# Kernel tuning notes

Measured on AMD Instinct MI355X. Metric: run time of the kernel, lower is better.

The kernel has to match this reference:

```python
import jax, jax.numpy as jnp
import numpy as np

DIM, SEQ, HEADS, HDIM, BATCH, VOCAB, NVOCAB = 512, 1024, 8, 64, 8, 1024, 3
EPS = 1e-5


def layer_norm(x, g, b):
    mu = x.mean(-1, keepdims=True)
    var = x.var(-1, keepdims=True)
    return (x - mu) * jax.lax.rsqrt(var + EPS) * g + b


def multiscale_retention(x, Wq, Wk, Wv, Wg, Wo):
    B, S, D = x.shape
    def split(h):  # [B,S,D] -> [B,H,S,hd]
        return h.reshape(B, S, HEADS, HDIM).transpose(0, 2, 1, 3)
    q, k, v = split(x @ Wq), split(x @ Wk), split(x @ Wv)
    # RetNet per-head decays and causal decay matrix D[h,n,m] = gamma_h^(n-m), n>=m
    gammas = 1.0 - 2.0 ** (-5.0 - jnp.arange(HEADS, dtype=jnp.float32))
    n = jnp.arange(S)
    diff = n[:, None] - n[None, :]
    decay = jnp.where(diff >= 0, gammas[:, None, None] ** jnp.maximum(diff, 0).astype(jnp.float32), 0.0)
    scores = jnp.einsum('bhsd,bhtd->bhst', q, k) * (1.0 / np.sqrt(HDIM))
    y = jnp.einsum('bhst,bhtd->bhsd', scores * decay, v)
    # group norm per head (no affine)
    mu = y.mean(-1, keepdims=True)
    var = y.var(-1, keepdims=True)
    y = (y - mu) * jax.lax.rsqrt(var + EPS)
    y = y.transpose(0, 2, 1, 3).reshape(B, S, D)
    gate = jax.nn.swish(x @ Wg)
    return (gate * y) @ Wo


def feed_forward(x, W1, b1, W2, b2):
    return jax.nn.relu(x @ W1 + b1) @ W2 + b2


def setup_inputs() -> dict:
    key = jax.random.key(0)
    ks = jax.random.split(key, 12)
    s = 0.02
    return {
        'ids': jax.random.randint(ks[0], (NVOCAB, BATCH, SEQ), 0, VOCAB),
        'emb_tables': jax.random.normal(ks[1], (NVOCAB, VOCAB, DIM), jnp.float32) * s,
        'pos_emb': jax.random.normal(ks[2], (NVOCAB, SEQ, DIM), jnp.float32) * s,
        'ln_gamma': jnp.ones((DIM,), jnp.float32),
        'ln_beta': jnp.zeros((DIM,), jnp.float32),
        'Wq': jax.random.normal(ks[3], (DIM, DIM), jnp.float32) * s,
        'Wk': jax.random.normal(ks[4], (DIM, DIM), jnp.float32) * s,
        'Wv': jax.random.normal(ks[5], (DIM, DIM), jnp.float32) * s,
        'Wg': jax.random.normal(ks[6], (DIM, DIM), jnp.float32) * s,
        'Wo': jax.random.normal(ks[7], (DIM, DIM), jnp.float32) * s,
        'W1': jax.random.normal(ks[8], (DIM, DIM), jnp.float32) * s,
        'b1': jnp.zeros((DIM,), jnp.float32),
        'W2': jax.random.normal(ks[9], (DIM, DIM), jnp.float32) * s,
        'b2': jnp.zeros((DIM,), jnp.float32),
        'fc_W': jax.random.normal(ks[10], (SEQ * DIM, 1), jnp.float32) * s,
        'fc_b': jnp.zeros((1,), jnp.float32),
    }


def reference(ids, emb_tables, pos_emb, ln_gamma, ln_beta, Wq, Wk, Wv, Wg, Wo,
              W1, b1, W2, b2, fc_W, fc_b):
    x = None
    for i in range(NVOCAB):  # loop over vocab embeddings, x overwritten each pass (as in source)
        emb = emb_tables[i][ids[i]] + pos_emb[i][None, :, :]  # [B,S,D]
        x = layer_norm(emb, ln_gamma, ln_beta)
        x = multiscale_retention(x, Wq, Wk, Wv, Wg, Wo) + x
        x = feed_forward(layer_norm(x, ln_gamma, ln_beta), W1, b1, W2, b2) + x
        x = layer_norm(x, ln_gamma, ln_beta)
    flat = x.reshape(x.shape[0], -1)  # Flatten
    return jax.nn.sigmoid(flat @ fc_W + fc_b)  # dropout inactive at inference
```

## Files before the change

### kernel.cpp

```cpp
#include <hip/hip_runtime.h>
#include <math.h>

typedef unsigned short u16;
typedef __attribute__((ext_vector_type(8))) _Float16 half8;
typedef __attribute__((ext_vector_type(4))) float f32x4;
typedef __attribute__((ext_vector_type(4))) unsigned short us4;


static __device__ __forceinline__ u16 f2h(float f) {
    _Float16 h = (_Float16)f;
    return __builtin_bit_cast(u16, h);
}
static __device__ __forceinline__ float h2f(u16 u) {
    return (float)__builtin_bit_cast(_Float16, u);
}
static __device__ __forceinline__ void gl_lds16(const void* g, void* l) {
    __builtin_amdgcn_global_load_lds(
        (const __attribute__((address_space(1))) void*)g,
        (__attribute__((address_space(3))) void*)l, 16, 0, 0);
}

__global__ __launch_bounds__(256) void prep_kernel(
    const float* __restrict__ Wq, const float* __restrict__ Wk, const float* __restrict__ Wv,
    const float* __restrict__ Wg, const float* __restrict__ Wo, const float* __restrict__ W1,
    const float* __restrict__ W2, u16* __restrict__ WT,
    const int* __restrict__ ids, const float* __restrict__ emb, const float* __restrict__ pos,
    const float* __restrict__ gam, const float* __restrict__ bet, u16* __restrict__ x0h)
{
    __shared__ float tile[64][65];
    int bx = blockIdx.x, t = threadIdx.x;
    if (bx < 448) {
        const float* Ws[7] = {Wq, Wk, Wv, Wg, Wo, W1, W2};
        int w = bx >> 6, rem = bx & 63;
        int k0 = (rem >> 3) * 64, n0 = (rem & 7) * 64;
        const float* W = Ws[w];
        for (int c = t; c < 4096; c += 256) {
            int row = c >> 6, col = c & 63;
            tile[row][col] = W[(size_t)(k0 + row) * 512 + n0 + col];
        }
        __syncthreads();
        for (int c = t; c < 4096; c += 256) {
            int row = c >> 6, col = c & 63;
            WT[(size_t)w * 262144 + (size_t)(n0 + row) * 512 + k0 + col] = f2h(tile[col][row]);
        }
    } else {
        int wid = t >> 6, lane = t & 63;
        int row = (bx - 448) * 4 + wid;
        int col = lane * 8;
        int id = ids[2 * 8192 + row];
        const float* e = emb + (size_t)(2 * 1024 + id) * 512 + col;
        const float* p = pos + (size_t)(2 * 1024 + (row & 1023)) * 512 + col;
        float4 e0 = *(const float4*)e, e1 = *(const float4*)(e + 4);
        float4 p0 = *(const float4*)p, p1 = *(const float4*)(p + 4);
        float v[8] = {e0.x + p0.x, e0.y + p0.y, e0.z + p0.z, e0.w + p0.w,
                      e1.x + p1.x, e1.y + p1.y, e1.z + p1.z, e1.w + p1.w};
        float s1 = 0.f, s2 = 0.f;
#pragma unroll
        for (int j = 0; j < 8; ++j) { s1 += v[j]; s2 += v[j] * v[j]; }
#pragma unroll
        for (int o = 32; o >= 1; o >>= 1) {
            s1 += __shfl_xor(s1, o, 64);
            s2 += __shfl_xor(s2, o, 64);
        }
        float mu = s1 * (1.f / 512.f);
        float var = fmaxf(s2 * (1.f / 512.f) - mu * mu, 0.f);
        float rs = 1.f / sqrtf(var + 1e-5f);
        float4 g0 = *(const float4*)&gam[col], g1 = *(const float4*)&gam[col + 4];
        float4 b0 = *(const float4*)&bet[col], b1 = *(const float4*)&bet[col + 4];
        float gv[8] = {g0.x, g0.y, g0.z, g0.w, g1.x, g1.y, g1.z, g1.w};
        float bv[8] = {b0.x, b0.y, b0.z, b0.w, b1.x, b1.y, b1.z, b1.w};
        half8 hv;
#pragma unroll
        for (int j = 0; j < 8; ++j) hv[j] = (_Float16)((v[j] - mu) * rs * gv[j] + bv[j]);
        *(half8*)&x0h[(size_t)row * 512 + col] = hv;
    }
}

__global__ __launch_bounds__(256) void ln_kernel(
    const u16* __restrict__ xin,
    const float* __restrict__ gam, const float* __restrict__ bet,
    u16* __restrict__ outh,
    const float* __restrict__ fcW, float* __restrict__ fcpart)
{
    int wid = threadIdx.x >> 6, lane = threadIdx.x & 63;
    int row = blockIdx.x * 4 + wid;
    int col = lane * 8;
    float v[8];
    half8 x = *(const half8*)&xin[(size_t)row * 512 + col];
#pragma unroll
    for (int j = 0; j < 8; ++j) v[j] = (float)x[j];
    float s1 = 0.f, s2 = 0.f;
#pragma unroll
    for (int j = 0; j < 8; ++j) { s1 += v[j]; s2 += v[j] * v[j]; }
#pragma unroll
    for (int o = 32; o >= 1; o >>= 1) {
        s1 += __shfl_xor(s1, o, 64);
        s2 += __shfl_xor(s2, o, 64);
    }
    float mu = s1 * (1.f / 512.f);
    float var = fmaxf(s2 * (1.f / 512.f) - mu * mu, 0.f);
    float rs = 1.f / sqrtf(var + 1e-5f);
    float4 g0 = *(const float4*)&gam[col], g1 = *(const float4*)&gam[col + 4];
    float4 b0 = *(const float4*)&bet[col], b1 = *(const float4*)&bet[col + 4];
    float gv[8] = {g0.x, g0.y, g0.z, g0.w, g1.x, g1.y, g1.z, g1.w};
    float bv[8] = {b0.x, b0.y, b0.z, b0.w, b1.x, b1.y, b1.z, b1.w};
    float y[8];
#pragma unroll
    for (int j = 0; j < 8; ++j) y[j] = (v[j] - mu) * rs * gv[j] + bv[j];
    if (outh) {
        half8 hv;
#pragma unroll
        for (int j = 0; j < 8; ++j) hv[j] = (_Float16)y[j];
        *(half8*)&outh[(size_t)row * 512 + col] = hv;
    }
    if (fcW) {
        int srow = row & 1023;
        const float* wp = &fcW[(size_t)srow * 512 + col];
        float4 w0 = *(const float4*)wp, w1 = *(const float4*)(wp + 4);
        float d = y[0] * w0.x + y[1] * w0.y + y[2] * w0.z + y[3] * w0.w +
                  y[4] * w1.x + y[5] * w1.y + y[6] * w1.z + y[7] * w1.w;
#pragma unroll
        for (int o = 32; o >= 1; o >>= 1) d += __shfl_xor(d, o, 64);
        if (lane == 0) fcpart[row] = d;
    }
}

static __device__ __forceinline__ void stage_tile(
    const u16* pa0, const u16* pa1, const u16* pb0, const u16* pb1,
    u16* ldsw, int slot, int kt)
{
    int off = kt * 32;
    u16* d = ldsw + slot * 16384;
    gl_lds16(pa0 + off, d);
    gl_lds16(pa1 + off, d + 4096);
    gl_lds16(pb0 + off, d + 8192);
    gl_lds16(pb1 + off, d + 12288);
}

static __device__ __forceinline__ void compute_tile(
    const u16* lds, int slot, int wm, int wn, int quad, int l15, f32x4 (&acc)[8][4])
{
    const u16* A = lds + slot * 16384;
    const u16* B = A + 8192;
    __builtin_amdgcn_s_setprio(1);
#pragma unroll
    for (int mq = 0; mq < 2; ++mq)
#pragma unroll
        for (int nq = 0; nq < 2; ++nq) {
            half8 a[4], b[2];
#pragma unroll
            for (int i = 0; i < 4; ++i)
                a[i] = *(const half8*)&A[(wm * 128 + mq * 64 + i * 16 + l15) * 32 + quad * 8];
#pragma unroll
            for (int j = 0; j < 2; ++j)
                b[j] = *(const half8*)&B[(wn * 64 + nq * 32 + j * 16 + l15) * 32 + quad * 8];
#pragma unroll
            for (int i = 0; i < 4; ++i)
#pragma unroll
                for (int j = 0; j < 2; ++j)
                    acc[mq * 4 + i][nq * 2 + j] = __builtin_amdgcn_mfma_f32_16x16x32_f16(
                        a[i], b[j], acc[mq * 4 + i][nq * 2 + j], 0, 0, 0);
        }
    __builtin_amdgcn_s_setprio(0);
}

#define QITER(KT, VM)                                                              \
    do {                                                                           \
        if ((KT) + 3 < 16) stage_tile(pa0, pa1, pb0, pb1, ldsw, ((KT) + 3) & 3, (KT) + 3); \
        asm volatile("s_waitcnt vmcnt(" #VM ")" ::: "memory");                     \
        __builtin_amdgcn_s_barrier();                                              \
        asm volatile("" ::: "memory");                                             \
        compute_tile(lds, (KT) & 3, wm, wn, quad, l15, acc);                       \
        asm volatile("" ::: "memory");                                             \
        __builtin_amdgcn_s_barrier();                                              \
    } while (0)

__global__ __launch_bounds__(512, 2) void gemm_f16(
    const u16* __restrict__ A2, const u16* __restrict__ Bg,
    u16* __restrict__ outh, int ostride)
{
    __shared__ u16 lds[65536];
    int t = threadIdx.x;
    int wid = t >> 6, lane = t & 63, quad = lane >> 4, l15 = lane & 15;
    int wm = wid >> 2, wn = wid & 3;
    int orig = blockIdx.x;
    int wgid = (orig & 7) * 32 + (orig >> 3);
    int m0 = (wgid >> 3) * 256, n0 = (wgid & 7) * 256;

    int srow = t >> 2, sc = (t & 3) * 8;
    const u16* pa0 = A2 + (size_t)(m0 + srow) * 512 + sc;
    const u16* pa1 = pa0 + (size_t)128 * 512;
    const u16* pb0 = Bg + (size_t)(n0 + srow) * 512 + sc;
    const u16* pb1 = pb0 + (size_t)128 * 512;
    u16* ldsw = lds + wid * 512;

    f32x4 acc[8][4];
#pragma unroll
    for (int i = 0; i < 8; ++i)
#pragma unroll
        for (int j = 0; j < 4; ++j) acc[i][j] = (f32x4){0.f, 0.f, 0.f, 0.f};

    stage_tile(pa0, pa1, pb0, pb1, ldsw, 0, 0);
    stage_tile(pa0, pa1, pb0, pb1, ldsw, 1, 1);
    stage_tile(pa0, pa1, pb0, pb1, ldsw, 2, 2);

    QITER(0, 12);  QITER(1, 12);  QITER(2, 12);  QITER(3, 12);
    QITER(4, 12);  QITER(5, 12);  QITER(6, 12);  QITER(7, 12);
    QITER(8, 12);  QITER(9, 12);  QITER(10, 12); QITER(11, 12);
    QITER(12, 12);
    QITER(13, 8);  QITER(14, 4);  QITER(15, 0);

    u16* C = lds;
#pragma unroll
    for (int i = 0; i < 8; ++i)
#pragma unroll
        for (int j = 0; j < 4; ++j)
#pragma unroll
            for (int r = 0; r < 4; ++r)
                C[(wm * 128 + i * 16 + quad * 4 + r) * 256 + wn * 64 + j * 16 + l15] =
                    f2h(acc[i][j][r]);
    __builtin_amdgcn_s_barrier();
    asm volatile("" ::: "memory");
#pragma unroll
    for (int it = 0; it < 16; ++it) {
        int idx = it * 512 + t;
        int row = idx >> 5, ch = idx & 31;
        *(half8*)&outh[(size_t)(m0 + row) * ostride + n0 + ch * 8] =
            *(const half8*)&C[row * 256 + ch * 8];
    }
}

static __device__ __forceinline__ void stage_n64(
    const u16* pa, const u16* pb, u16* ldsw, int slot, int kt)
{
    int off = kt * 32;
    u16* d = ldsw + slot * 8192;
    gl_lds16(pa + off, d);
    gl_lds16(pb + off, d + 4096);
}

static __device__ __forceinline__ void compute_n64(
    const u16* lds, int slot, int wm, int wn, int quad, int l15, f32x4 (&acc)[4][2])
{
    const u16* A = lds + slot * 8192;
    const u16* B = A + 4096;
    __builtin_amdgcn_s_setprio(1);
    half8 a[4], b[2];
#pragma unroll
    for (int i = 0; i < 4; ++i)
        a[i] = *(const half8*)&A[(wm * 64 + i * 16 + l15) * 32 + quad * 8];
#pragma unroll
    for (int j = 0; j < 2; ++j)
        b[j] = *(const half8*)&B[(wn * 32 + j * 16 + l15) * 32 + quad * 8];
#pragma unroll
    for (int i = 0; i < 4; ++i)
#pragma unroll
        for (int j = 0; j < 2; ++j)
            acc[i][j] = __builtin_amdgcn_mfma_f32_16x16x32_f16(a[i], b[j], acc[i][j], 0, 0, 0);
    __builtin_amdgcn_s_setprio(0);
}

#define NITER(KT, VM)                                                          \
    do {                                                                       \
        if ((KT) + 3 < 16) stage_n64(pa, pb, ldsw, ((KT) + 3) & 3, (KT) + 3);  \
        asm volatile("s_waitcnt vmcnt(" #VM ")" ::: "memory");                 \
        __builtin_amdgcn_s_barrier();                                          \
        asm volatile("" ::: "memory");                                         \
        compute_n64(lds, (KT) & 3, wm, wn, quad, l15, acc);                    \
        asm volatile("" ::: "memory");                                         \
        __builtin_amdgcn_s_barrier();                                          \
    } while (0)

__global__ __launch_bounds__(512, 2) void gemm_f16_n64(
    const u16* __restrict__ A2, const u16* __restrict__ Bg,
    u16* __restrict__ outh,
    const u16* __restrict__ res, const float* __restrict__ bias, int mode)
{
    __shared__ u16 lds[32768];
    int t = threadIdx.x;
    int wid = t >> 6, lane = t & 63, quad = lane >> 4, l15 = lane & 15;
    int wm = wid >> 2, wn = wid & 3;
    int orig = blockIdx.x;
    int wgid = (orig & 7) * 32 + (orig >> 3);
    int m0 = (wgid >> 2) * 128, n0 = (wgid & 3) * 128;

    int srow = t >> 2, sc = (t & 3) * 8;
    const u16* pa = A2 + (size_t)(m0 + srow) * 512 + sc;
    const u16* pb = Bg + (size_t)(n0 + srow) * 512 + sc;
    u16* ldsw = lds + wid * 512;

    f32x4 acc[4][2];
#pragma unroll
    for (int i = 0; i < 4; ++i)
#pragma unroll
        for (int j = 0; j < 2; ++j) acc[i][j] = (f32x4){0.f, 0.f, 0.f, 0.f};

    stage_n64(pa, pb, ldsw, 0, 0);
    stage_n64(pa, pb, ldsw, 1, 1);
    stage_n64(pa, pb, ldsw, 2, 2);

    NITER(0, 6);  NITER(1, 6);  NITER(2, 6);  NITER(3, 6);
    NITER(4, 6);  NITER(5, 6);  NITER(6, 6);  NITER(7, 6);
    NITER(8, 6);  NITER(9, 6);  NITER(10, 6); NITER(11, 6);
    NITER(12, 6);
    NITER(13, 4); NITER(14, 2); NITER(15, 0);

#pragma unroll
    for (int i = 0; i < 4; ++i)
#pragma unroll
        for (int j = 0; j < 2; ++j) {
            int nl = wn * 32 + j * 16 + l15;
            int n = n0 + nl;
#pragma unroll
            for (int r = 0; r < 4; ++r) {
                int rl = wm * 64 + i * 16 + quad * 4 + r;
                int m = m0 + rl;
                float v = acc[i][j][r];
                if (mode == 1) v += h2f(res[(size_t)m * 512 + n]);
                else if (mode == 2) v = fmaxf(v + bias[n], 0.f);
                else if (mode == 3) v += bias[n] + h2f(res[(size_t)m * 512 + n]);
                lds[rl * 128 + nl] = f2h(v);
            }
        }
    __builtin_amdgcn_s_barrier();
    asm volatile("" ::: "memory");
#pragma unroll
    for (int it = 0; it < 4; ++it) {
        int idx = it * 512 + t;
        int row = idx >> 4, ch = idx & 15;
        *(half8*)&outh[(size_t)(m0 + row) * 512 + n0 + ch * 8] =
            *(const half8*)&lds[row * 128 + ch * 8];
    }
}

__global__ __launch_bounds__(256) void chunk_t(
    const u16* __restrict__ QKVGh, u16* __restrict__ Tst)
{
    __shared__ u16 kth[64 * 144];
    __shared__ u16 vth[64 * 144];
    int t = threadIdx.x;
    int wid = t >> 6, lane = t & 63, quad = lane >> 4, l15 = lane & 15;
    int bh = blockIdx.x >> 3, c = blockIdx.x & 7;
    int b = bh >> 3, h = bh & 7;
    float gamma = 1.f - exp2f(-(float)(5 + h));
    float l2g = log2f(gamma);

    for (int cc = t; cc < 2048; cc += 256) {
        int d = cc & 63, mseg = cc >> 6;
        size_t gbase = (size_t)(b * 1024 + c * 128 + mseg * 4) * 2048 + h * 64 + d;
        us4 k4, v4;
#pragma unroll
        for (int i = 0; i < 4; ++i) {
            float kv = h2f(QKVGh[gbase + 512 + (size_t)i * 2048]);
            k4[i] = f2h(kv * exp2f((float)(127 - (mseg * 4 + i)) * l2g));
            v4[i] = QKVGh[gbase + 1024 + (size_t)i * 2048];
        }
        int base = d * 144 + (((mseg >> 1) + d) & 15) * 8 + (mseg & 1) * 4;
        *(us4*)&kth[base] = k4;
        *(us4*)&vth[base] = v4;
    }
    __syncthreads();
    f32x4 T[4];
#pragma unroll
    for (int dt = 0; dt < 4; ++dt) T[dt] = (f32x4){0.f, 0.f, 0.f, 0.f};
    int ra = wid * 16 + l15;
#pragma unroll
    for (int ks = 0; ks < 4; ++ks) {
        half8 av = *(const half8*)&vth[ra * 144 + ((ks * 4 + quad + ra) & 15) * 8];
#pragma unroll
        for (int dt = 0; dt < 4; ++dt) {
            int rb = dt * 16 + l15;
            half8 bk = *(const half8*)&kth[rb * 144 + ((ks * 4 + quad + rb) & 15) * 8];
            T[dt] = __builtin_amdgcn_mfma_f32_16x16x32_f16(av, bk, T[dt], 0, 0, 0);
        }
    }
#pragma unroll
    for (int dt = 0; dt < 4; ++dt)
#pragma unroll
        for (int r = 0; r < 4; ++r) {
            int i = wid * 16 + quad * 4 + r;
            int j = dt * 16 + l15;
            Tst[(((size_t)bh * 8 + c) * 64 + i) * 64 + j] = f2h(T[dt][r]);
        }
}

__global__ __launch_bounds__(256) void retention_f16(
    const u16* __restrict__ QKVGh, const u16* __restrict__ Tst, u16* __restrict__ Zh)
{
    __shared__ u16 kh[128 * 64];
    __shared__ u16 vth[64 * 144];
    __shared__ u16 ph[4][16 * 132];

    int t = threadIdx.x;
    int wid = t >> 6, lane = t & 63, quad = lane >> 4, l15 = lane & 15;
    int bh = blockIdx.x >> 3, qt = blockIdx.x & 7;
    int b = bh >> 3, h = bh & 7;
    int n0 = qt * 128;

    float gamma = 1.f - exp2f(-(float)(5 + h));
    float l2g = log2f(gamma);

    {
        int srow = wid * 8 + (lane >> 3);
        int scol = (lane & 7) * 8;
#pragma unroll
        for (int i = 0; i < 4; ++i) {
            int r = i * 32 + srow;
            gl_lds16(&QKVGh[(size_t)(b * 1024 + n0 + r) * 2048 + 512 + h * 64 + scol],
                     &kh[(i * 32 + wid * 8) * 64]);
        }
    }
    for (int c = t; c < 2048; c += 256) {
        int d = c & 63, mseg = c >> 6;
        size_t gbase = (size_t)(b * 1024 + n0 + mseg * 4) * 2048 + 1024 + h * 64 + d;
        us4 v4 = {QKVGh[gbase], QKVGh[gbase + 2048],
                  QKVGh[gbase + 4096], QKVGh[gbase + 6144]};
        int base = d * 144 + (((mseg >> 1) + d) & 15) * 8 + (mseg & 1) * 4;
        *(us4*)&vth[base] = v4;
    }

    half8 aH[2][2], aHs[2][2];
#pragma unroll
    for (int g = 0; g < 2; ++g) {
        int rowloc = wid * 32 + g * 16 + l15;
        int qrow = b * 1024 + n0 + rowloc;
        const u16* qp = QKVGh + (size_t)qrow * 2048 + h * 64;
        float qs = exp2f((float)(rowloc + 1) * l2g - 3.f);
#pragma unroll
        for (int ks = 0; ks < 2; ++ks) {
            aH[g][ks] = *(const half8*)&qp[ks * 32 + quad * 8];
#pragma unroll
            for (int j = 0; j < 8; ++j)
                aHs[g][ks][j] = (_Float16)((float)aH[g][ks][j] * qs);
        }
    }

    half8 sf[2][4];
    if (qt > 0) {
        float sa[2][4][8];
#pragma unroll
        for (int ks = 0; ks < 2; ++ks)
#pragma unroll
            for (int dt = 0; dt < 4; ++dt)
#pragma unroll
                for (int j = 0; j < 8; ++j) sa[ks][dt][j] = 0.f;
        for (int c = 0; c < qt; ++c) {
            float sc = exp2f((float)(128 * (qt - 1 - c)) * l2g);
            const u16* tp = &Tst[((size_t)bh * 8 + c) * 4096];
#pragma unroll
            for (int ks = 0; ks < 2; ++ks)
#pragma unroll
                for (int dt = 0; dt < 4; ++dt) {
                    half8 tv = *(const half8*)&tp[(dt * 16 + l15) * 64 + ks * 32 + quad * 8];
#pragma unroll
                    for (int j = 0; j < 8; ++j) sa[ks][dt][j] += sc * (float)tv[j];
                }
        }
#pragma unroll
        for (int ks = 0; ks < 2; ++ks)
#pragma unroll
            for (int dt = 0; dt < 4; ++dt)
#pragma unroll
                for (int j = 0; j < 8; ++j) sf[ks][dt][j] = (_Float16)sa[ks][dt][j];
    }
    __syncthreads();

    f32x4 yacc[2][4];
#pragma unroll
    for (int g = 0; g < 2; ++g)
#pragma unroll
        for (int dt = 0; dt < 4; ++dt) yacc[g][dt] = (f32x4){0.f, 0.f, 0.f, 0.f};

    if (qt > 0) {
#pragma unroll
        for (int ks = 0; ks < 2; ++ks)
#pragma unroll
            for (int g = 0; g < 2; ++g)
#pragma unroll
                for (int dt = 0; dt < 4; ++dt)
                    yacc[g][dt] = __builtin_amdgcn_mfma_f32_16x16x32_f16(aHs[g][ks], sf[ks][dt], yacc[g][dt], 0, 0, 0);
    }

#pragma unroll
    for (int g = 0; g < 2; ++g) {
        f32x4 sacc[8];
#pragma unroll
        for (int tn = 0; tn < 8; ++tn) sacc[tn] = (f32x4){0.f, 0.f, 0.f, 0.f};
#pragma unroll
        for (int tn = 0; tn < 8; ++tn)
#pragma unroll
            for (int ks = 0; ks < 2; ++ks) {
                half8 bH = *(const half8*)&kh[(tn * 16 + l15) * 64 + ks * 32 + quad * 8];
                sacc[tn] = __builtin_amdgcn_mfma_f32_16x16x32_f16(aH[g][ks], bH, sacc[tn], 0, 0, 0);
            }
#pragma unroll
        for (int tn = 0; tn < 8; ++tn) {
            int mloc = tn * 16 + l15;
#pragma unroll
            for (int r = 0; r < 4; ++r) {
                int nloc = wid * 32 + g * 16 + quad * 4 + r;
                int diff = nloc - mloc;
                float p = (diff >= 0) ? sacc[tn][r] * exp2f((float)diff * l2g - 3.0f) : 0.f;
                ph[wid][(quad * 4 + r) * 132 + tn * 16 + l15] = f2h(p);
            }
        }
        half8 pH[4];
#pragma unroll
        for (int ks = 0; ks < 4; ++ks)
            pH[ks] = *(const half8*)&ph[wid][l15 * 132 + ks * 32 + quad * 8];
#pragma unroll
        for (int dt = 0; dt < 4; ++dt) {
            int d = dt * 16 + l15;
#pragma unroll
            for (int ks = 0; ks < 4; ++ks) {
                half8 vv = *(const half8*)&vth[d * 144 + ((ks * 4 + quad + d) & 15) * 8];
                yacc[g][dt] = __builtin_amdgcn_mfma_f32_16x16x32_f16(pH[ks], vv, yacc[g][dt], 0, 0, 0);
            }
        }
    }

#pragma unroll
    for (int g = 0; g < 2; ++g) {
#pragma unroll
        for (int r = 0; r < 4; ++r) {
            float s1 = yacc[g][0][r] + yacc[g][1][r] + yacc[g][2][r] + yacc[g][3][r];
            float s2 = yacc[g][0][r] * yacc[g][0][r] + yacc[g][1][r] * yacc[g][1][r] +
                       yacc[g][2][r] * yacc[g][2][r] + yacc[g][3][r] * yacc[g][3][r];
#pragma unroll
            for (int o = 1; o <= 8; o <<= 1) {
                s1 += __shfl_xor(s1, o, 64);
                s2 += __shfl_xor(s2, o, 64);
            }
            float mu = s1 * (1.f / 64.f);
            float var = fmaxf(s2 * (1.f / 64.f) - mu * mu, 0.f);
            float rs = 1.f / sqrtf(var + 1e-5f);
            int nglob = n0 + wid * 32 + g * 16 + quad * 4 + r;
            size_t grow = (size_t)(b * 1024 + nglob);
#pragma unroll
            for (int dt = 0; dt < 4; ++dt) {
                int d = dt * 16 + l15;
                float yv = (yacc[g][dt][r] - mu) * rs;
                float gt = h2f(QKVGh[grow * 2048 + 1536 + h * 64 + d]);
                float sw = gt / (1.f + expf(-gt));
                Zh[grow * 512 + h * 64 + d] = f2h(yv * sw);
            }
        }
    }
}

__global__ __launch_bounds__(256) void fc_final(const float* __restrict__ fcpart,
                                                const float* __restrict__ fcb,
                                                float* __restrict__ out)
{
    __shared__ float red[4];
    int b = blockIdx.x, t = threadIdx.x;
    float4 v = *(const float4*)&fcpart[(size_t)b * 1024 + t * 4];
    float s = v.x + v.y + v.z + v.w;
    int wid = t >> 6, lane = t & 63;
#pragma unroll
    for (int o = 32; o >= 1; o >>= 1) s += __shfl_xor(s, o, 64);
    if (lane == 0) red[wid] = s;
    __syncthreads();
    if (t == 0) {
        float l = red[0] + red[1] + red[2] + red[3] + fcb[0];
        out[b] = 1.f / (1.f + expf(-l));
    }
}

extern "C" void kernel_launch(void* const* d_in, const int* in_sizes, int n_in,
                              void* d_out, int out_size, void* d_ws, size_t ws_size,
                              hipStream_t stream)
{
    const int* ids = (const int*)d_in[0];
    const float* emb = (const float*)d_in[1];
    const float* pos = (const float*)d_in[2];
    const float* ln_g = (const float*)d_in[3];
    const float* ln_b = (const float*)d_in[4];
    const float* Wq = (const float*)d_in[5];
    const float* Wk = (const float*)d_in[6];
    const float* Wv = (const float*)d_in[7];
    const float* Wg = (const float*)d_in[8];
    const float* Wo = (const float*)d_in[9];
    const float* W1 = (const float*)d_in[10];
    const float* b1 = (const float*)d_in[11];
    const float* W2 = (const float*)d_in[12];
    const float* b2 = (const float*)d_in[13];
    const float* fcW = (const float*)d_in[14];
    const float* fcb = (const float*)d_in[15];
    float* out = (float*)d_out;

    char* ws = (char*)d_ws;
    u16* WT     = (u16*)(ws);
    u16* x0h    = (u16*)(ws + 3670016);
    u16* Zh     = (u16*)(ws + 12058624);
    u16* QKVGh  = (u16*)(ws + 20447232);
    float* fcpart = (float*)(ws + 54001664);
    u16* Tst    = (u16*)(ws + 54034432);
    u16* X1h = QKVGh;
    u16* Th  = (u16*)((char*)QKVGh + 8388608);
    u16* Hh  = (u16*)((char*)QKVGh + 16777216);
    u16* X2h = Zh;

    prep_kernel<<<2496, 256, 0, stream>>>(Wq, Wk, Wv, Wg, Wo, W1, W2, WT,
                                          ids, emb, pos, ln_g, ln_b, x0h);
    gemm_f16<<<256, 512, 0, stream>>>(x0h, WT, QKVGh, 2048);
    chunk_t<<<512, 256, 0, stream>>>(QKVGh, Tst);
    retention_f16<<<512, 256, 0, stream>>>(QKVGh, Tst, Zh);
    gemm_f16_n64<<<256, 512, 0, stream>>>(Zh, WT + 4 * 262144, X1h, x0h, nullptr, 1);
    ln_kernel<<<2048, 256, 0, stream>>>(X1h, ln_g, ln_b, Th, nullptr, nullptr);
    gemm_f16_n64<<<256, 512, 0, stream>>>(Th, WT + 5 * 262144, Hh, nullptr, b1, 2);
    gemm_f16_n64<<<256, 512, 0, stream>>>(Hh, WT + 6 * 262144, X2h, X1h, b2, 3);
    ln_kernel<<<2048, 256, 0, stream>>>(X2h, ln_g, ln_b, nullptr, fcW, fcpart);
    fc_final<<<8, 256, 0, stream>>>(fcpart, fcb, out);
}
```

Measured before the change: 210.2 us.

## Fold layer norms into GEMM epilogues via row statistics and weight prescaling

Removes both standalone layernorm kernels. The Wo GEMM epilogue accumulates per-row sum and sum-of-squares with atomics. The W1 GEMM then applies the normalisation algebraically, using gamma folded into W1 plus precomputed column sums of gamma*W1 and beta*W1. The final GEMM no longer writes X2; it accumulates row stats and a dot with gamma*fcW, and fc_final reconstructs the normalised FC sum. This saves two memory-bound passes and intermediate writes, at the cost of atomics, extra prep work, and possible precision loss from computing variance as E[x²]−mu² on the unnormalised GEMM input.

```diff
diff --git a/kernel.cpp b/kernel.cpp
--- a/kernel.cpp
+++ b/kernel.cpp
@@ -25,7 +25,14 @@
     const float* __restrict__ Wg, const float* __restrict__ Wo, const float* __restrict__ W1,
     const float* __restrict__ W2, u16* __restrict__ WT,
     const int* __restrict__ ids, const float* __restrict__ emb, const float* __restrict__ pos,
-    const float* __restrict__ gam, const float* __restrict__ bet, u16* __restrict__ x0h)
+    const float* __restrict__ gam, const float* __restrict__ bet, u16* __restrict__ x0h,
+    const float* __restrict__ fcW,
+    float* __restrict__ statz,
+    float* __restrict__ fcP,
+    float* __restrict__ sW1g,
+    float* __restrict__ gfcW,
+    float* __restrict__ Gfc,
+    float* __restrict__ Bfc)
 {
     __shared__ float tile[64][65];
     int bx = blockIdx.x, t = threadIdx.x;
@@ -41,9 +48,11 @@
         __syncthreads();
         for (int c = t; c < 4096; c += 256) {
             int row = c >> 6, col = c & 63;
-            WT[(size_t)w * 262144 + (size_t)(n0 + row) * 512 + k0 + col] = f2h(tile[col][row]);
-        }
-    } else {
+            float sc = (w == 5) ? gam[k0 + col] : 1.f;
+            WT[(size_t)w * 262144 + (size_t)(n0 + row) * 512 + k0 + col] =
+                f2h(tile[col][row] * sc);
+        }
+    } else if (bx < 2496) {
         int wid = t >> 6, lane = t & 63;
         int row = (bx - 448) * 4 + wid;
         int col = lane * 8;
@@ -73,55 +82,48 @@
 #pragma unroll
         for (int j = 0; j < 8; ++j) hv[j] = (_Float16)((v[j] - mu) * rs * gv[j] + bv[j]);
         *(half8*)&x0h[(size_t)row * 512 + col] = hv;
-    }
-}
-
-__global__ __launch_bounds__(256) void ln_kernel(
-    const u16* __restrict__ xin,
-    const float* __restrict__ gam, const float* __restrict__ bet,
-    u16* __restrict__ outh,
-    const float* __restrict__ fcW, float* __restrict__ fcpart)
-{
-    int wid = threadIdx.x >> 6, lane = threadIdx.x & 63;
-    int row = blockIdx.x * 4 + wid;
-    int col = lane * 8;
-    float v[8];
-    half8 x = *(const half8*)&xin[(size_t)row * 512 + col];
-#pragma unroll
-    for (int j = 0; j < 8; ++j) v[j] = (float)x[j];
-    float s1 = 0.f, s2 = 0.f;
-#pragma unroll
-    for (int j = 0; j < 8; ++j) { s1 += v[j]; s2 += v[j] * v[j]; }
-#pragma unroll
-    for (int o = 32; o >= 1; o >>= 1) {
-        s1 += __shfl_xor(s1, o, 64);
-        s2 += __shfl_xor(s2, o, 64);
-    }
-    float mu = s1 * (1.f / 512.f);
-    float var = fmaxf(s2 * (1.f / 512.f) - mu * mu, 0.f);
-    float rs = 1.f / sqrtf(var + 1e-5f);
-    float4 g0 = *(const float4*)&gam[col], g1 = *(const float4*)&gam[col + 4];
-    float4 b0 = *(const float4*)&bet[col], b1 = *(const float4*)&bet[col + 4];
-    float gv[8] = {g0.x, g0.y, g0.z, g0.w, g1.x, g1.y, g1.z, g1.w};
-    float bv[8] = {b0.x, b0.y, b0.z, b0.w, b1.x, b1.y, b1.z, b1.w};
-    float y[8];
-#pragma unroll
-    for (int j = 0; j < 8; ++j) y[j] = (v[j] - mu) * rs * gv[j] + bv[j];
-    if (outh) {
-        half8 hv;
-#pragma unroll
-        for (int j = 0; j < 8; ++j) hv[j] = (_Float16)y[j];
-        *(half8*)&outh[(size_t)row * 512 + col] = hv;
-    }
-    if (fcW) {
-        int srow = row & 1023;
-        const float* wp = &fcW[(size_t)srow * 512 + col];
-        float4 w0 = *(const float4*)wp, w1 = *(const float4*)(wp + 4);
-        float d = y[0] * w0.x + y[1] * w0.y + y[2] * w0.z + y[3] * w0.w +
-                  y[4] * w1.x + y[5] * w1.y + y[6] * w1.z + y[7] * w1.w;
-#pragma unroll
-        for (int o = 32; o >= 1; o >>= 1) d += __shfl_xor(d, o, 64);
-        if (lane == 0) fcpart[row] = d;
+    } else if (bx < 2504) {
+        int idx = (bx - 2496) * 256 + t;
+        for (int i = idx; i < 32768; i += 2048) statz[i] = 0.f;
+        for (int i = idx; i < 8192; i += 2048) fcP[i] = 0.f;
+    } else if (bx < 2512) {
+        int j = bx - 2504;
+        int n = j * 64 + (t & 63), kq = t >> 6;
+        float sg = 0.f, sb = 0.f;
+        for (int k = kq * 128; k < kq * 128 + 128; ++k) {
+            float w = W1[(size_t)k * 512 + n];
+            sg += gam[k] * w;
+            sb += bet[k] * w;
+        }
+        float* sh = &tile[0][0];
+        sh[kq * 64 + (t & 63)] = sg;
+        sh[256 + kq * 64 + (t & 63)] = sb;
+        __syncthreads();
+        if (t < 64) {
+            float g4 = sh[t] + sh[64 + t] + sh[128 + t] + sh[192 + t];
+            float b4 = sh[256 + t] + sh[320 + t] + sh[384 + t] + sh[448 + t];
+            sW1g[j * 64 + t] = g4;
+            sW1g[512 + j * 64 + t] = b4;
+        }
+    } else {
+        int j = bx - 2512;
+        int srow = j * 128 + (t >> 1);
+        int k0 = (t & 1) * 256;
+        const float* fr = fcW + (size_t)srow * 512 + k0;
+        float* gw = gfcW + (size_t)srow * 512 + k0;
+        float G = 0.f, B = 0.f;
+        for (int k = 0; k < 256; k += 4) {
+            float4 f = *(const float4*)(fr + k);
+            float4 g4 = *(const float4*)(gam + k0 + k);
+            float4 b4 = *(const float4*)(bet + k0 + k);
+            float4 gf = {g4.x * f.x, g4.y * f.y, g4.z * f.z, g4.w * f.w};
+            *(float4*)(gw + k) = gf;
+            G += gf.x + gf.y + gf.z + gf.w;
+            B += b4.x * f.x + b4.y * f.y + b4.z * f.z + b4.w * f.w;
+        }
+        G += __shfl_xor(G, 1, 64);
+        B += __shfl_xor(B, 1, 64);
+        if ((t & 1) == 0) { Gfc[srow] = G; Bfc[srow] = B; }
     }
 }
 
@@ -274,7 +276,10 @@
 __global__ __launch_bounds__(512, 2) void gemm_f16_n64(
     const u16* __restrict__ A2, const u16* __restrict__ Bg,
     u16* __restrict__ outh,
-    const u16* __restrict__ res, const float* __restrict__ bias, int mode)
+    const u16* __restrict__ res, const float* __restrict__ bias, int mode,
+    float* __restrict__ statw, const float* __restrict__ statr,
+    const float* __restrict__ sW1g, const float* __restrict__ gfcW,
+    float* __restrict__ fcP)
 {
     __shared__ u16 lds[32768];
     int t = threadIdx.x;
@@ -305,31 +310,93 @@
     NITER(12, 6);
     NITER(13, 4); NITER(14, 2); NITER(15, 0);
 
-#pragma unroll
-    for (int i = 0; i < 4; ++i)
-#pragma unroll
-        for (int j = 0; j < 2; ++j) {
-            int nl = wn * 32 + j * 16 + l15;
-            int n = n0 + nl;
+    float rsv[4][4], muv[4][4];
+    if (mode == 4) {
+#pragma unroll
+        for (int i = 0; i < 4; ++i)
+#pragma unroll
+            for (int r = 0; r < 4; ++r) {
+                int m = m0 + wm * 64 + i * 16 + quad * 4 + r;
+                float s1 = statr[m], s2 = statr[m + 8192];
+                float mu = s1 * (1.f / 512.f);
+                float var = fmaxf(s2 * (1.f / 512.f) - mu * mu, 0.f);
+                rsv[i][r] = 1.f / sqrtf(var + 1e-5f);
+                muv[i][r] = mu;
+            }
+    }
+#pragma unroll
+    for (int j = 0; j < 2; ++j) {
+        int nl = wn * 32 + j * 16 + l15;
+        int n = n0 + nl;
+        float swn = 0.f, cbn = 0.f, bn = 0.f;
+        if (mode == 4) { swn = sW1g[n]; cbn = sW1g[512 + n] + bias[n]; }
+        else if (mode == 5) bn = bias[n];
+#pragma unroll
+        for (int i = 0; i < 4; ++i)
 #pragma unroll
             for (int r = 0; r < 4; ++r) {
                 int rl = wm * 64 + i * 16 + quad * 4 + r;
                 int m = m0 + rl;
                 float v = acc[i][j][r];
                 if (mode == 1) v += h2f(res[(size_t)m * 512 + n]);
-                else if (mode == 2) v = fmaxf(v + bias[n], 0.f);
-                else if (mode == 3) v += bias[n] + h2f(res[(size_t)m * 512 + n]);
+                else if (mode == 4) {
+                    float rs = rsv[i][r];
+                    v = fmaxf(fmaf(rs, v, fmaf(-muv[i][r] * rs, swn, cbn)), 0.f);
+                } else {
+                    v += bn + h2f(res[(size_t)m * 512 + n]);
+                }
                 lds[rl * 128 + nl] = f2h(v);
             }
-        }
+    }
     __builtin_amdgcn_s_barrier();
     asm volatile("" ::: "memory");
-#pragma unroll
-    for (int it = 0; it < 4; ++it) {
-        int idx = it * 512 + t;
-        int row = idx >> 4, ch = idx & 15;
-        *(half8*)&outh[(size_t)(m0 + row) * 512 + n0 + ch * 8] =
-            *(const half8*)&lds[row * 128 + ch * 8];
+    if (mode != 5) {
+#pragma unroll
+        for (int it = 0; it < 4; ++it) {
+            int idx = it * 512 + t;
+            int row = idx >> 4, ch = idx & 15;
+            *(half8*)&outh[(size_t)(m0 + row) * 512 + n0 + ch * 8] =
+                *(const half8*)&lds[row * 128 + ch * 8];
+        }
+    }
+    if (mode != 4) {
+        int row = t >> 2, q = t & 3;
+        int m = m0 + row;
+        const u16* lr = &lds[row * 128 + q * 32];
+        float s1 = 0.f, s2 = 0.f, P = 0.f;
+        if (mode == 5) {
+            const float* gp = &gfcW[(size_t)(m & 1023) * 512 + n0 + q * 32];
+#pragma unroll
+            for (int c = 0; c < 4; ++c) {
+                half8 hv = *(const half8*)&lr[c * 8];
+                float4 ga = *(const float4*)&gp[c * 8];
+                float4 gb = *(const float4*)&gp[c * 8 + 4];
+                float gv[8] = {ga.x, ga.y, ga.z, ga.w, gb.x, gb.y, gb.z, gb.w};
+#pragma unroll
+                for (int jj = 0; jj < 8; ++jj) {
+                    float x = (float)hv[jj];
+                    s1 += x; s2 += x * x; P += x * gv[jj];
+                }
+            }
+        } else {
+#pragma unroll
+            for (int c = 0; c < 4; ++c) {
+                half8 hv = *(const half8*)&lr[c * 8];
+#pragma unroll
+                for (int jj = 0; jj < 8; ++jj) {
+                    float x = (float)hv[jj];
+                    s1 += x; s2 += x * x;
+                }
+            }
+        }
+        s1 += __shfl_xor(s1, 1, 64); s1 += __shfl_xor(s1, 2, 64);
+        s2 += __shfl_xor(s2, 1, 64); s2 += __shfl_xor(s2, 2, 64);
+        if (mode == 5) { P += __shfl_xor(P, 1, 64); P += __shfl_xor(P, 2, 64); }
+        if (q == 0) {
+            atomicAdd(&statw[m], s1);
+            atomicAdd(&statw[m + 8192], s2);
+            if (mode == 5) atomicAdd(&fcP[m], P);
+        }
     }
 }
 
@@ -548,14 +615,28 @@
     }
 }
 
-__global__ __launch_bounds__(256) void fc_final(const float* __restrict__ fcpart,
-                                                const float* __restrict__ fcb,
-                                                float* __restrict__ out)
+__global__ __launch_bounds__(256) void fc_final(
+    const float* __restrict__ stat2, const float* __restrict__ fcP,
+    const float* __restrict__ Gfc, const float* __restrict__ Bfc,
+    const float* __restrict__ fcb, float* __restrict__ out)
 {
     __shared__ float red[4];
     int b = blockIdx.x, t = threadIdx.x;
-    float4 v = *(const float4*)&fcpart[(size_t)b * 1024 + t * 4];
-    float s = v.x + v.y + v.z + v.w;
+    int r0 = b * 1024 + t * 4;
+    float Pa[4], s1a[4], s2a[4], Ga[4], Ba[4];
+    *(float4*)Pa = *(const float4*)&fcP[r0];
+    *(float4*)s1a = *(const float4*)&stat2[r0];
+    *(float4*)s2a = *(const float4*)&stat2[r0 + 8192];
+    *(float4*)Ga = *(const float4*)&Gfc[t * 4];
+    *(float4*)Ba = *(const float4*)&Bfc[t * 4];
+    float s = 0.f;
+#pragma unroll
+    for (int j = 0; j < 4; ++j) {
+        float mu = s1a[j] * (1.f / 512.f);
+        float var = fmaxf(s2a[j] * (1.f / 512.f) - mu * mu, 0.f);
+        float rs = 1.f / sqrtf(var + 1e-5f);
+        s += rs * Pa[j] - mu * rs * Ga[j] + Ba[j];
+    }
     int wid = t >> 6, lane = t & 63;
 #pragma unroll
     for (int o = 32; o >= 1; o >>= 1) s += __shfl_xor(s, o, 64);
@@ -594,22 +675,28 @@
     u16* x0h    = (u16*)(ws + 3670016);
     u16* Zh     = (u16*)(ws + 12058624);
     u16* QKVGh  = (u16*)(ws + 20447232);
-    float* fcpart = (float*)(ws + 54001664);
+    float* fcP  = (float*)(ws + 54001664);
     u16* Tst    = (u16*)(ws + 54034432);
+    float* stat1 = (float*)(ws + 58228736);
+    float* stat2 = (float*)(ws + 58294272);
+    float* sW1g  = (float*)(ws + 58359808);
+    float* Gfc   = (float*)(ws + 58363904);
+    float* Bfc   = (float*)(ws + 58368000);
+    float* gfcW  = (float*)(ws + 58372096);
     u16* X1h = QKVGh;
-    u16* Th  = (u16*)((char*)QKVGh + 8388608);
     u16* Hh  = (u16*)((char*)QKVGh + 16777216);
-    u16* X2h = Zh;
-
-    prep_kernel<<<2496, 256, 0, stream>>>(Wq, Wk, Wv, Wg, Wo, W1, W2, WT,
-                                          ids, emb, pos, ln_g, ln_b, x0h);
+
+    prep_kernel<<<2520, 256, 0, stream>>>(Wq, Wk, Wv, Wg, Wo, W1, W2, WT,
+                                          ids, emb, pos, ln_g, ln_b, x0h,
+                                          fcW, stat1, fcP, sW1g, gfcW, Gfc, Bfc);
     gemm_f16<<<256, 512, 0, stream>>>(x0h, WT, QKVGh, 2048);
     chunk_t<<<512, 256, 0, stream>>>(QKVGh, Tst);
     retention_f16<<<512, 256, 0, stream>>>(QKVGh, Tst, Zh);
-    gemm_f16_n64<<<256, 512, 0, stream>>>(Zh, WT + 4 * 262144, X1h, x0h, nullptr, 1);
-    ln_kernel<<<2048, 256, 0, stream>>>(X1h, ln_g, ln_b, Th, nullptr, nullptr);
-    gemm_f16_n64<<<256, 512, 0, stream>>>(Th, WT + 5 * 262144, Hh, nullptr, b1, 2);
-    gemm_f16_n64<<<256, 512, 0, stream>>>(Hh, WT + 6 * 262144, X2h, X1h, b2, 3);
-    ln_kernel<<<2048, 256, 0, stream>>>(X2h, ln_g, ln_b, nullptr, fcW, fcpart);
-    fc_final<<<8, 256, 0, stream>>>(fcpart, fcb, out);
-}
+    gemm_f16_n64<<<256, 512, 0, stream>>>(Zh, WT + 4 * 262144, X1h, x0h, nullptr, 1,
+                                          stat1, nullptr, nullptr, nullptr, nullptr);
+    gemm_f16_n64<<<256, 512, 0, stream>>>(X1h, WT + 5 * 262144, Hh, nullptr, b1, 4,
+                                          nullptr, stat1, sW1g, nullptr, nullptr);
+    gemm_f16_n64<<<256, 512, 0, stream>>>(Hh, WT + 6 * 262144, nullptr, X1h, b2, 5,
+                                          stat2, nullptr, nullptr, gfcW, fcP);
+    fc_final<<<8, 256, 0, stream>>>(stat2, fcP, Gfc, Bfc, fcb, out);
+}
```

Result: slower. 228.2 us (+8.5%).
